# Kernel optimization log

Hardware: AMD Instinct MI355X
Metric: run time of the kernel (lower is better)

## Reference

```python
import jax, jax.numpy as jnp
import numpy as np

HIDDEN = 2048
NUM_HEADS = 16
HEAD_DIM = HIDDEN // NUM_HEADS
WORLD_SIZE = 4
BATCH = 1
SEQ_SHARD = 2048


def setup_inputs() -> dict:
    key = jax.random.key(0)
    ks = jax.random.split(key, 9)
    s = 1.0 / np.sqrt(HIDDEN)
    return {
        'hidden_states': jax.random.normal(ks[0], (BATCH, SEQ_SHARD, HIDDEN), jnp.float32),
        'wq': jax.random.normal(ks[1], (HIDDEN, HIDDEN), jnp.float32) * s,
        'bq': jax.random.normal(ks[2], (HIDDEN,), jnp.float32) * s,
        'wk': jax.random.normal(ks[3], (HIDDEN, HIDDEN), jnp.float32) * s,
        'bk': jax.random.normal(ks[4], (HIDDEN,), jnp.float32) * s,
        'wv': jax.random.normal(ks[5], (HIDDEN, HIDDEN), jnp.float32) * s,
        'bv': jax.random.normal(ks[6], (HIDDEN,), jnp.float32) * s,
        'wo': jax.random.normal(ks[7], (HIDDEN, HIDDEN), jnp.float32) * s,
        'bo': jax.random.normal(ks[8], (HIDDEN,), jnp.float32) * s,
    }


def _ring_attention(q, k, v):
    # q, k, v: [B, H, S, D]. Simulation: every ring step receives the SAME
    # local KV shard (all_k_shards are clones of k), accumulated with
    # flash-style online softmax across WORLD_SIZE steps.
    B, H, S, D = q.shape
    scale = 1.0 / np.sqrt(D)
    output_acc = jnp.zeros_like(q)
    max_score = jnp.full((B, H, S, 1), -jnp.inf, dtype=q.dtype)
    sum_exp = jnp.zeros((B, H, S, 1), dtype=q.dtype)
    for _ in range(WORLD_SIZE):  # fixed small loop over ring steps
        scores = jnp.einsum('bhsd,bhtd->bhst', q, k) * scale  # [B,H,S,S]
        new_max = jnp.max(scores, axis=-1, keepdims=True)
        combined_max = jnp.maximum(max_score, new_max)
        old_scale = jnp.exp(max_score - combined_max)
        new_scale = jnp.exp(new_max - combined_max)
        new_exp = jnp.exp(scores - new_max)
        sum_exp = sum_exp * old_scale + jnp.sum(new_exp, axis=-1, keepdims=True) * new_scale
        output_acc = output_acc * old_scale + jnp.einsum('bhst,bhtd->bhsd', new_exp, v) * new_scale
        max_score = combined_max
    return output_acc / sum_exp


def reference(hidden_states, wq, bq, wk, bk, wv, bv, wo, bo):
    B, S, _ = hidden_states.shape
    # nn.Linear: y = x @ W^T + b
    q = hidden_states @ wq.T + bq
    k = hidden_states @ wk.T + bk
    v = hidden_states @ wv.T + bv
    split = lambda t: t.reshape(B, S, NUM_HEADS, HEAD_DIM).transpose(0, 2, 1, 3)
    attn = _ring_attention(split(q), split(k), split(v))  # [B,H,S,D]
    attn = attn.transpose(0, 2, 1, 3).reshape(B, S, HIDDEN)
    return attn @ wo.T + bo
```

## Files before the change

kernel.cpp:

```cpp
#include <hip/hip_runtime.h>
#include <hip/hip_bf16.h>
#include <stdint.h>

#define SEQ 2048
#define HID 2048
#define NH 16
#define HD 128
#define QSCALE_L2E 0.1275304429019769f

typedef __attribute__((ext_vector_type(4))) float f32x4;
typedef __attribute__((ext_vector_type(8))) short short8;
typedef __attribute__((ext_vector_type(4))) float f4;
typedef __attribute__((ext_vector_type(4))) unsigned short us4;

__device__ __forceinline__ unsigned short f2bu(float f) {
  union { float f; unsigned int u; } c; c.f = f;
  unsigned int u = c.u + 0x7fffu + ((c.u >> 16) & 1u);
  return (unsigned short)(u >> 16);
}

__device__ __forceinline__ unsigned short f2bu_fast(float f) {
  union { float f; unsigned int u; } c; c.f = f;
  return (unsigned short)((c.u + 0x8000u) >> 16);
}

__device__ __forceinline__ float b2f(unsigned short u) {
  union { unsigned int u; float f; } c; c.u = ((unsigned int)u) << 16; return c.f;
}

__device__ __forceinline__ float exp2fast(float x) {
  float r; asm("v_exp_f32 %0, %1" : "=v"(r) : "v"(x)); return r;
}

__device__ __forceinline__ void gload_lds16(const void* g, void* l) {
  __builtin_amdgcn_global_load_lds((const __attribute__((address_space(1))) void*)g,
                                   (__attribute__((address_space(3))) void*)l, 16, 0, 0);
}

#define BAR() __builtin_amdgcn_s_barrier()
#define LGKM0() do { asm volatile("s_waitcnt lgkmcnt(0)" ::: "memory"); __builtin_amdgcn_sched_barrier(0); } while (0)
#define VM6()   do { asm volatile("s_waitcnt vmcnt(6)"   ::: "memory"); __builtin_amdgcn_sched_barrier(0); } while (0)
#define VM0()   do { asm volatile("s_waitcnt vmcnt(0)"   ::: "memory"); __builtin_amdgcn_sched_barrier(0); } while (0)

__global__ __launch_bounds__(256) void cvt_kernel(
    const float* __restrict__ s0, const float* __restrict__ s1,
    const float* __restrict__ s2, const float* __restrict__ s3,
    const float* __restrict__ s4,
    unsigned short* __restrict__ d0, unsigned short* __restrict__ d1,
    unsigned short* __restrict__ d2, unsigned short* __restrict__ d3,
    unsigned short* __restrict__ d4, int n)
{
  const float* s; unsigned short* d;
  switch (blockIdx.y) {
    case 0: s = s0; d = d0; break;
    case 1: s = s1; d = d1; break;
    case 2: s = s2; d = d2; break;
    case 3: s = s3; d = d3; break;
    default: s = s4; d = d4; break;
  }
  const int stride = gridDim.x * blockDim.x;
  for (int i = blockIdx.x * blockDim.x + threadIdx.x; i * 8 < n; i += stride) {
    f4 v0 = *(const f4*)&s[i * 8];
    f4 v1 = *(const f4*)&s[i * 8 + 4];
    short8 o;
    o[0] = (short)f2bu(v0[0]); o[1] = (short)f2bu(v0[1]);
    o[2] = (short)f2bu(v0[2]); o[3] = (short)f2bu(v0[3]);
    o[4] = (short)f2bu(v1[0]); o[5] = (short)f2bu(v1[1]);
    o[6] = (short)f2bu(v1[2]); o[7] = (short)f2bu(v1[3]);
    *(short8*)&d[i * 8] = o;
  }
}

template<int MODE>
__global__ __launch_bounds__(256, 2) void gemm128(
    const unsigned short* __restrict__ A,
    const unsigned short* __restrict__ B,
    const float* __restrict__ b0, const float* __restrict__ b1, const float* __restrict__ b2,
    unsigned short* __restrict__ O0, unsigned short* __restrict__ O1, unsigned short* __restrict__ O2,
    float* __restrict__ Of, int M, int N, int K)
{
  constexpr int ASZ = 64 * 64;
  constexpr int BSZ = 128 * 64;

  extern __shared__ unsigned short lds[];
  const int tid = threadIdx.x;
  const int lane = tid & 63, w = tid >> 6;
  const int g = lane >> 4, q = lane & 15;
  const long bm = (long)blockIdx.y * 64, bn = (long)blockIdx.x * 128;
  const int NK = K >> 6;

  const int srl = lane >> 3;
  const int scE = ((lane & 7) ^ srl) * 8;
  const int c0 = (g ^ (q & 7)) * 8;
  const int c1 = c0 ^ 32;
  const int aB = q * 64;
  const int bB = (w * 32 + q) * 64;

  f32x4 acc[4][2] = {};
  short8 a[4][2], b[2][2];

#define STAGE_A(jj) do {                                                      \
    unsigned short* dst_ = lds + (((jj) & 1) ? ASZ : 0);                      \
    _Pragma("unroll")                                                         \
    for (int c_ = 0; c_ < 2; ++c_) {                                          \
      const long row_ = (c_ * 4 + w) * 8 + srl;                               \
      gload_lds16(&A[(bm + row_) * (long)K + (jj) * 64 + scE],                \
                  &dst_[(c_ * 4 + w) * 512]);                                 \
    }                                                                         \
  } while (0)

#define STAGE_B(jj) do {                                                      \
    unsigned short* dst_ = lds + 2 * ASZ + (((jj) & 1) ? BSZ : 0);            \
    _Pragma("unroll")                                                         \
    for (int c_ = 0; c_ < 4; ++c_) {                                          \
      const long row_ = (c_ * 4 + w) * 8 + srl;                               \
      gload_lds16(&B[(bn + row_) * (long)K + (jj) * 64 + scE],                \
                  &dst_[(c_ * 4 + w) * 512]);                                 \
    }                                                                         \
  } while (0)

#define QUAD8(ni)                                                             \
  do {                                                                        \
    __builtin_amdgcn_s_setprio(1);                                            \
    _Pragma("unroll")                                                         \
    for (int mi_ = 0; mi_ < 4; ++mi_) {                                       \
      acc[mi_][ni] = __builtin_amdgcn_mfma_f32_16x16x32_bf16(                 \
          a[mi_][0], b[ni][0], acc[mi_][ni], 0, 0, 0);                        \
      acc[mi_][ni] = __builtin_amdgcn_mfma_f32_16x16x32_bf16(                 \
          a[mi_][1], b[ni][1], acc[mi_][ni], 0, 0, 0);                        \
    }                                                                         \
    __builtin_amdgcn_s_setprio(0);                                            \
  } while (0)

  STAGE_A(0); STAGE_B(0);
  STAGE_A(1); STAGE_B(1);
  VM6();
  BAR();

  for (int j = 0; j < NK; ++j) {
    unsigned short* At = lds + ((j & 1) ? ASZ : 0);
    unsigned short* Bt = lds + 2 * ASZ + ((j & 1) ? BSZ : 0);

#pragma unroll
    for (int mi = 0; mi < 4; ++mi) {
      a[mi][0] = *(const short8*)&At[aB + mi * 1024 + c0];
      a[mi][1] = *(const short8*)&At[aB + mi * 1024 + c1];
    }
#pragma unroll
    for (int ni = 0; ni < 2; ++ni) {
      b[ni][0] = *(const short8*)&Bt[bB + ni * 1024 + c0];
      b[ni][1] = *(const short8*)&Bt[bB + ni * 1024 + c1];
    }
    QUAD8(0);
    LGKM0();
    BAR();
    if (j + 2 < NK) { STAGE_A(j + 2); STAGE_B(j + 2); }
    QUAD8(1);
    if (j < NK - 2) { VM6(); } else { VM0(); }
    BAR();
  }

#pragma unroll
  for (int ni = 0; ni < 2; ++ni) {
    const int col = (int)bn + w * 32 + ni * 16 + q;
    float bv;
    if (MODE == 4) {
      const int which = col >> 11, c = col & 2047;
      const float* bp = which == 0 ? b0 : (which == 1 ? b1 : b2);
      bv = bp[c];
    } else {
      bv = b0[col];
    }
#pragma unroll
    for (int mi = 0; mi < 4; ++mi)
#pragma unroll
      for (int r = 0; r < 4; ++r) {
        const long row = bm + mi * 16 + 4 * g + r;
        const float v = acc[mi][ni][r] + bv;
        if (MODE == 4) {
          const int which = col >> 11, c = col & 2047, head = c >> 7, d = c & 127;
          if (which == 0)      O0[((long)head * SEQ + row) * HD + d] = f2bu(v * QSCALE_L2E);
          else if (which == 1) O1[((long)head * SEQ + row) * HD + d] = f2bu(v);
          else                 O2[((long)head * HD + d) * SEQ + row] = f2bu(v);
        } else {
          Of[row * (long)N + col] = v;
        }
      }
  }
#undef STAGE_A
#undef STAGE_B
#undef QUAD8
}

#define KVB 64
__global__ __launch_bounds__(256) void flash_attn(
    const unsigned short* __restrict__ Qb,
    const unsigned short* __restrict__ Kb,
    const unsigned short* __restrict__ VTb,
    unsigned short* __restrict__ attnb)
{
  __shared__ __align__(16) unsigned short Kt[64 * 128];
  __shared__ __align__(16) unsigned short Vt[128 * 64];
  __shared__ __align__(16) unsigned short Pt[4][16 * 64];
  const int tid = threadIdx.x;
  const int l = tid & 63, w = tid >> 6;
  const int g = l >> 4, q = l & 15;
  const int h = blockIdx.y, qb = blockIdx.x;
  const int qrow0 = qb * 64 + w * 16;

  short8 qf[4];
#pragma unroll
  for (int dc = 0; dc < 4; ++dc)
    qf[dc] = *(const short8*)&Qb[((long)h * SEQ + qrow0 + q) * HD + dc * 32 + g * 8];

  f32x4 oacc[8] = {};
  float lsum[4] = {0.f, 0.f, 0.f, 0.f};

  const int kr = tid >> 4, kc16 = tid & 15;
  const int vr = tid >> 3, vc8 = tid & 7;
  const unsigned short* Kg = Kb + (long)h * SEQ * HD;
  const unsigned short* Vg = VTb + (long)h * HD * SEQ;

  short8 kreg[4], vreg[4];
#pragma unroll
  for (int it = 0; it < 4; ++it) {
    kreg[it] = *(const short8*)&Kg[(long)(kr + it * 16) * HD + kc16 * 8];
    vreg[it] = *(const short8*)&Vg[(long)(vr + it * 32) * SEQ + vc8 * 8];
  }

  for (int kb = 0; kb < SEQ; kb += KVB) {
    __syncthreads();
#pragma unroll
    for (int it = 0; it < 4; ++it) {
      const int krow = kr + it * 16;
      *(short8*)&Kt[((krow * 256 + kc16 * 16) ^ ((krow & 7) << 4)) >> 1] = kreg[it];
      const int vrow = vr + it * 32;
      *(short8*)&Vt[((vrow * 128 + vc8 * 16) ^ ((vrow & 7) << 4)) >> 1] = vreg[it];
    }
    __syncthreads();
    if (kb + KVB < SEQ) {
#pragma unroll
      for (int it = 0; it < 4; ++it) {
        kreg[it] = *(const short8*)&Kg[(long)(kb + KVB + kr + it * 16) * HD + kc16 * 8];
        vreg[it] = *(const short8*)&Vg[(long)(vr + it * 32) * SEQ + kb + KVB + vc8 * 8];
      }
    }

    f32x4 sacc[4] = {};
#pragma unroll
    for (int kc = 0; kc < 4; ++kc) {
      const int krow = kc * 16 + q;
      const int sw = (krow & 7) << 4;
#pragma unroll
      for (int dc = 0; dc < 4; ++dc) {
        short8 kf = *(const short8*)&Kt[((krow * 256 + dc * 64 + g * 16) ^ sw) >> 1];
        sacc[kc] = __builtin_amdgcn_mfma_f32_16x16x32_bf16(qf[dc], kf, sacc[kc], 0, 0, 0);
      }
    }

    float p[4][4];
#pragma unroll
    for (int r = 0; r < 4; ++r) {
#pragma unroll
      for (int kc = 0; kc < 4; ++kc) p[kc][r] = exp2fast(sacc[kc][r]);
      lsum[r] += (p[0][r] + p[1][r]) + (p[2][r] + p[3][r]);
    }

    unsigned short* Pw = &Pt[w][0];
#pragma unroll
    for (int r = 0; r < 4; ++r) {
      const int prow = 4 * g + r;
      const int sw = (prow & 7) << 4;
#pragma unroll
      for (int kc = 0; kc < 4; ++kc)
        Pw[((prow * 128 + (kc * 16 + q) * 2) ^ sw) >> 1] = f2bu_fast(p[kc][r]);
    }

    short8 pf[2];
    const int psw = (q & 7) << 4;
#pragma unroll
    for (int ks = 0; ks < 2; ++ks)
      pf[ks] = *(const short8*)&Pw[((q * 128 + ks * 64 + g * 16) ^ psw) >> 1];
#pragma unroll
    for (int dt = 0; dt < 8; ++dt) {
      const int vrow = dt * 16 + q;
#pragma unroll
      for (int ks = 0; ks < 2; ++ks) {
        short8 vf = *(const short8*)&Vt[((vrow * 128 + ks * 64 + g * 16) ^ psw) >> 1];
        oacc[dt] = __builtin_amdgcn_mfma_f32_16x16x32_bf16(pf[ks], vf, oacc[dt], 0, 0, 0);
      }
    }
  }

#pragma unroll
  for (int off = 1; off < 16; off <<= 1)
#pragma unroll
    for (int r = 0; r < 4; ++r) lsum[r] += __shfl_xor(lsum[r], off);

  const float rl0 = 1.f / lsum[0], rl1 = 1.f / lsum[1];
  const float rl2 = 1.f / lsum[2], rl3 = 1.f / lsum[3];
#pragma unroll
  for (int dt = 0; dt < 8; ++dt) {
    const long colb = (long)h * HD + dt * 16 + q;
    attnb[(long)(qrow0 + 4 * g + 0) * HID + colb] = f2bu(oacc[dt][0] * rl0);
    attnb[(long)(qrow0 + 4 * g + 1) * HID + colb] = f2bu(oacc[dt][1] * rl1);
    attnb[(long)(qrow0 + 4 * g + 2) * HID + colb] = f2bu(oacc[dt][2] * rl2);
    attnb[(long)(qrow0 + 4 * g + 3) * HID + colb] = f2bu(oacc[dt][3] * rl3);
  }
}

extern "C" void kernel_launch(void* const* d_in, const int* in_sizes, int n_in,
                              void* d_out, int out_size, void* d_ws, size_t ws_size,
                              hipStream_t stream)
{
  const float* x  = (const float*)d_in[0];
  const float* wq = (const float*)d_in[1];
  const float* bq = (const float*)d_in[2];
  const float* wk = (const float*)d_in[3];
  const float* bk = (const float*)d_in[4];
  const float* wv = (const float*)d_in[5];
  const float* bv = (const float*)d_in[6];
  const float* wo = (const float*)d_in[7];
  const float* bo = (const float*)d_in[8];

  const long NEL = (long)HID * HID;
  unsigned short* Xb   = (unsigned short*)d_ws;
  unsigned short* Wqkv = Xb + NEL;
  unsigned short* Wob  = Wqkv + 3 * NEL;
  unsigned short* Qbuf = Wob + NEL;
  unsigned short* Kbuf = Qbuf + NEL;
  unsigned short* VTb  = Kbuf + NEL;
  unsigned short* Attn = VTb + NEL;

  cvt_kernel<<<dim3(512, 5), 256, 0, stream>>>(
      x, wq, wk, wv, wo, Xb, Wqkv, Wqkv + NEL, Wqkv + 2 * NEL, Wob, (int)NEL);

  gemm128<4><<<dim3(48, 32), 256, 49152, stream>>>(
      Xb, Wqkv, bq, bk, bv, Qbuf, Kbuf, VTb, nullptr, SEQ, 3 * HID, HID);

  flash_attn<<<dim3(SEQ / 64, NH), 256, 0, stream>>>(Qbuf, Kbuf, VTb, Attn);

  gemm128<3><<<dim3(16, 32), 256, 49152, stream>>>(
      Attn, Wob, bo, nullptr, nullptr, nullptr, nullptr, nullptr,
      (float*)d_out, SEQ, HID, HID);
}
```

Before: 176.4 us.

## Replace QKV projection GEMM with 128x128-tile single-buffered kernel

Adds a new GEMM kernel that gives each block a 128x128 output tile, arranged as a 2x2 grid of waves each computing 64x64 with 16x16x32 bf16 MFMAs. It uses a single LDS stage of 32 KB and launch bounds allowing three blocks per CU. The QKV projection now launches half as many blocks along M as the old 64x128-tile double-buffered kernel. The larger tile is meant to raise operand reuse and cut global/LDS traffic per FLOP. In exchange it gives up load/compute overlap within a block, relying on occupancy instead, and leaves fewer blocks to fill the CUs.

```diff
diff --git a/kernel.cpp b/kernel.cpp
--- a/kernel.cpp
+++ b/kernel.cpp
@@ -72,6 +72,109 @@
 }
 
 template<int MODE>
+__global__ __launch_bounds__(256, 3) void gemm97(
+    const unsigned short* __restrict__ A,
+    const unsigned short* __restrict__ B,
+    const float* __restrict__ b0, const float* __restrict__ b1, const float* __restrict__ b2,
+    unsigned short* __restrict__ O0, unsigned short* __restrict__ O1, unsigned short* __restrict__ O2,
+    float* __restrict__ Of, int M, int N, int K)
+{
+  extern __shared__ unsigned short lds[];
+  const int tid = threadIdx.x;
+  const int lane = tid & 63, w = tid >> 6;
+  const int g = lane >> 4, q = lane & 15;
+  const int wgM = w >> 1, wgN = w & 1;
+  const long bm = (long)blockIdx.y * 128, bn = (long)blockIdx.x * 128;
+  const int NK = K >> 6;
+
+  const int srl = lane >> 3;
+  const int scE = ((lane & 7) ^ srl) * 8;
+  const int c0 = (g ^ (q & 7)) * 8;
+  const int c1 = c0 ^ 32;
+  const int aB = (wgM * 64 + q) * 64;
+  const int bB = (wgN * 64 + q) * 64;
+
+  f32x4 acc[4][4] = {};
+  short8 a[4][2], b[4][2];
+
+#define STAGE(gp, gbase, jj, ldsOff) do {                                     \
+    _Pragma("unroll")                                                         \
+    for (int c_ = 0; c_ < 4; ++c_) {                                          \
+      const long row_ = (c_ * 4 + w) * 8 + srl;                               \
+      gload_lds16(&(gp)[((gbase) + row_) * (long)K + (jj) * 64 + scE],        \
+                  &lds[(ldsOff) + (c_ * 4 + w) * 512]);                       \
+    }                                                                         \
+  } while (0)
+
+#define QUADD(n0, n1)                                                         \
+  do {                                                                        \
+    __builtin_amdgcn_s_setprio(1);                                            \
+    _Pragma("unroll")                                                         \
+    for (int mi_ = 0; mi_ < 4; ++mi_) {                                       \
+      acc[mi_][n0] = __builtin_amdgcn_mfma_f32_16x16x32_bf16(                 \
+          a[mi_][0], b[n0][0], acc[mi_][n0], 0, 0, 0);                        \
+      acc[mi_][n0] = __builtin_amdgcn_mfma_f32_16x16x32_bf16(                 \
+          a[mi_][1], b[n0][1], acc[mi_][n0], 0, 0, 0);                        \
+      acc[mi_][n1] = __builtin_amdgcn_mfma_f32_16x16x32_bf16(                 \
+          a[mi_][0], b[n1][0], acc[mi_][n1], 0, 0, 0);                        \
+      acc[mi_][n1] = __builtin_amdgcn_mfma_f32_16x16x32_bf16(                 \
+          a[mi_][1], b[n1][1], acc[mi_][n1], 0, 0, 0);                        \
+    }                                                                         \
+    __builtin_amdgcn_s_setprio(0);                                            \
+  } while (0)
+
+  for (int j = 0; j < NK; ++j) {
+    STAGE(A, bm, j, 0);
+    STAGE(B, bn, j, 8192);
+    VM0();
+    BAR();
+#pragma unroll
+    for (int mi = 0; mi < 4; ++mi) {
+      a[mi][0] = *(const short8*)&lds[aB + mi * 1024 + c0];
+      a[mi][1] = *(const short8*)&lds[aB + mi * 1024 + c1];
+    }
+#pragma unroll
+    for (int ni = 0; ni < 4; ++ni) {
+      b[ni][0] = *(const short8*)&lds[8192 + bB + ni * 1024 + c0];
+      b[ni][1] = *(const short8*)&lds[8192 + bB + ni * 1024 + c1];
+    }
+    QUADD(0, 1);
+    QUADD(2, 3);
+    BAR();
+  }
+
+#pragma unroll
+  for (int ni = 0; ni < 4; ++ni) {
+    const int col = (int)bn + wgN * 64 + ni * 16 + q;
+    float bv;
+    if (MODE == 4) {
+      const int which = col >> 11, c = col & 2047;
+      const float* bp = which == 0 ? b0 : (which == 1 ? b1 : b2);
+      bv = bp[c];
+    } else {
+      bv = b0[col];
+    }
+#pragma unroll
+    for (int mi = 0; mi < 4; ++mi)
+#pragma unroll
+      for (int r = 0; r < 4; ++r) {
+        const long row = bm + wgM * 64 + mi * 16 + 4 * g + r;
+        const float v = acc[mi][ni][r] + bv;
+        if (MODE == 4) {
+          const int which = col >> 11, c = col & 2047, head = c >> 7, d = c & 127;
+          if (which == 0)      O0[((long)head * SEQ + row) * HD + d] = f2bu(v * QSCALE_L2E);
+          else if (which == 1) O1[((long)head * SEQ + row) * HD + d] = f2bu(v);
+          else                 O2[((long)head * HD + d) * SEQ + row] = f2bu(v);
+        } else {
+          Of[row * (long)N + col] = v;
+        }
+      }
+  }
+#undef STAGE
+#undef QUADD
+}
+
+template<int MODE>
 __global__ __launch_bounds__(256, 2) void gemm128(
     const unsigned short* __restrict__ A,
     const unsigned short* __restrict__ B,
@@ -335,7 +438,7 @@
   cvt_kernel<<<dim3(512, 5), 256, 0, stream>>>(
       x, wq, wk, wv, wo, Xb, Wqkv, Wqkv + NEL, Wqkv + 2 * NEL, Wob, (int)NEL);
 
-  gemm128<4><<<dim3(48, 32), 256, 49152, stream>>>(
+  gemm97<4><<<dim3(48, 16), 256, 32768, stream>>>(
       Xb, Wqkv, bq, bk, bv, Qbuf, Kbuf, VTb, nullptr, SEQ, 3 * HID, HID);
 
   flash_attn<<<dim3(SEQ / 64, NH), 256, 0, stream>>>(Qbuf, Kbuf, VTb, Attn);
```

Measured after the change: 165.2 us. 1.07x faster.
